# Kernel optimization log

Hardware: AMD Instinct MI355X
Metric: run time of the kernel (lower is better)

The kernel has to match this reference:

```python
import jax, jax.numpy as jnp
import numpy as np

DT = 0.02
Z_DIM = 32
U_DIM = 16


def _mlp(x, layers):
    # layers: list of (W, b); SiLU between all but last layer
    n = len(layers)
    for i, (W, b) in enumerate(layers):
        x = x @ W + b
        if i < n - 1:
            x = jax.nn.silu(x)
    return x


def _forward(x, u,
             e_w1, e_b1, e_w2, e_b2, e_w3, e_b3,
             d_w1, d_b1, d_w2, d_b2, d_w3, d_b3, d_w4, d_b4,
             a_w1, a_b1, a_w2, a_b2, a_w3, a_b3,
             b_w1, b_b1, b_w2, b_b2, b_w3, b_b3):
    # encode
    z = _mlp(x, [(e_w1, e_b1), (e_w2, e_b2), (e_w3, e_b3)])          # (B, Z)
    # state-dependent A(x) parameters: pairs (a_i, b_i) per 2x2 block
    aux = _mlp(x, [(a_w1, a_b1), (a_w2, a_b2), (a_w3, a_b3)])        # (B, Z)
    a = aux[:, 0::2]                                                  # (B, Z/2)
    b = aux[:, 1::2]
    f = jnp.exp(a * DT)
    c = jnp.cos(b * DT)
    s = jnp.sin(b * DT)
    # A(x) @ z without materializing block-diagonal: per-pair rotation-scale
    z0 = z[:, 0::2]
    z1 = z[:, 1::2]
    Az = jnp.stack([f * (c * z0 - s * z1), f * (s * z0 + c * z1)], axis=-1).reshape(z.shape)
    # B(x) @ u
    Bmat = _mlp(x, [(b_w1, b_b1), (b_w2, b_b2), (b_w3, b_b3)]).reshape(-1, Z_DIM, U_DIM)
    Bu = jnp.einsum('bzu,bu->bz', Bmat, u)
    # latent Euler step + decode
    z_next = z + DT * (Az + Bu)
    return _mlp(z_next, [(d_w1, d_b1), (d_w2, d_b2), (d_w3, d_b3), (d_w4, d_b4)])


def setup_inputs() -> dict:
    key = jax.random.key(0)
    ks = iter(jax.random.split(key, 32))
    def w(shape, scale=0.02):
        return jax.random.normal(next(ks), shape, jnp.float32) * scale
    B, X, U, Z, H, A = 16384, 64, 16, 32, 1024, 256
    return {
        'x': jax.random.normal(next(ks), (B, X), jnp.float32),
        'u': jax.random.normal(next(ks), (B, U), jnp.float32),
        'e_w1': w((X, H)), 'e_b1': w((H,)),
        'e_w2': w((H, H)), 'e_b2': w((H,)),
        'e_w3': w((H, Z)), 'e_b3': w((Z,)),
        'd_w1': w((Z, H)), 'd_b1': w((H,)),
        'd_w2': w((H, H)), 'd_b2': w((H,)),
        'd_w3': w((H, H)), 'd_b3': w((H,)),
        'd_w4': w((H, X)), 'd_b4': w((X,)),
        'a_w1': w((X, A)), 'a_b1': w((A,)),
        'a_w2': w((A, A)), 'a_b2': w((A,)),
        'a_w3': w((A, Z)), 'a_b3': w((Z,)),
        'b_w1': w((X, A)), 'b_b1': w((A,)),
        'b_w2': w((A, A)), 'b_b2': w((A,)),
        'b_w3': w((A, Z * U)), 'b_b3': w((Z * U,)),
    }


def reference(x, u,
              e_w1, e_b1, e_w2, e_b2, e_w3, e_b3,
              d_w1, d_b1, d_w2, d_b2, d_w3, d_b3, d_w4, d_b4,
              a_w1, a_b1, a_w2, a_b2, a_w3, a_b3,
              b_w1, b_b1, b_w2, b_b2, b_w3, b_b3):
    return _forward(x, u,
                    e_w1, e_b1, e_w2, e_b2, e_w3, e_b3,
                    d_w1, d_b1, d_w2, d_b2, d_w3, d_b3, d_w4, d_b4,
                    a_w1, a_b1, a_w2, a_b2, a_w3, a_b3,
                    b_w1, b_b1, b_w2, b_b2, b_w3, b_b3)
```

## Files before the change

### kernel.cpp

```cpp
#include <hip/hip_runtime.h>
#include <cstdint>
#include <cstddef>

#define B_SZ 16384
#define X_D  64
#define U_D  16
#define Z_D  32
#define H_D  1024
#define A_D  256
#define DT_C 0.02f

typedef _Float16 f16;
typedef f16   f16x8 __attribute__((ext_vector_type(8)));
typedef f16   f16x4 __attribute__((ext_vector_type(4)));
typedef float f32x4 __attribute__((ext_vector_type(4)));
typedef float f32x16 __attribute__((ext_vector_type(16)));

#define AS1 __attribute__((address_space(1)))
#define AS3 __attribute__((address_space(3)))

__device__ __forceinline__ void gld_lds16(const void* g, void* l) {
    __builtin_amdgcn_global_load_lds((AS1 void*)(g), (AS3 void*)(l), 16, 0, 0);
}

#define BARX()  do { asm volatile("" ::: "memory"); __builtin_amdgcn_s_barrier(); \
                     asm volatile("" ::: "memory"); } while (0)
#define LGK0()  do { asm volatile("s_waitcnt lgkmcnt(0)" ::: "memory"); \
                     __builtin_amdgcn_sched_barrier(0); } while (0)
#define WAITV0() asm volatile("s_waitcnt vmcnt(0)" ::: "memory")

struct GArg {
    const f16*  A;
    const f16*  W;
    const float* bias;
    void*       C;
    int lda, ldc, K;
};
struct GSet { GArg g[3]; int yn0, yn1; };

template<int BM,int BN,int BK,int WM,int WN,bool SILU,int OM>
__launch_bounds__(256)
__global__ void gemm_k(GSet p)
{
    static_assert(OM != 1 || BN == 128, "OM1 repack assumes BN=128");
    int yb = blockIdx.y, gi = 0;
    if (yb >= p.yn0) { yb -= p.yn0; gi = 1; if (yb >= p.yn1) { yb -= p.yn1; gi = 2; } }
    const GArg ga = p.g[gi];

    constexpr int SEGROW = BK / 8;
    constexpr int SMASK  = (SEGROW < 8 ? SEGROW : 8) - 1;
    constexpr int WTM = BM / WM, WTN = BN / WN;
    static_assert(WTM % 32 == 0 && WTN % 32 == 0, "wave tile in 32x32 units");
    constexpr int RM = WTM / 32, RN = WTN / 32;
    constexpr int KS = BK / 16;
    constexpr int ITA = (BM * SEGROW) / 256;
    constexpr int ITB = (BN * SEGROW) / 256;

    constexpr int STAGE_B = (BM + BN) * BK * 2;
    constexpr int CS_B    = (OM == 1) ? BM * BN * 2 : 0;
    constexpr int SMEM_B  = STAGE_B > CS_B ? STAGE_B : CS_B;
    __shared__ __align__(16) char smem[SMEM_B];
    f16* As = (f16*)smem;
    f16* Bs = As + BM * BK;

    const int tid  = threadIdx.x;
    const int lane = tid & 63;
    const int wave = tid >> 6;
    const int wm = wave / WN, wn = wave % WN;
    const int l31 = lane & 31, half = lane >> 5;

    const size_t arow0 = (size_t)blockIdx.x * BM;
    const size_t brow0 = (size_t)yb * BN;
    const int lda = ga.lda, K = ga.K;

    const f16* aptr[ITA];
    const f16* bptr[ITB];
#pragma unroll
    for (int it = 0; it < ITA; ++it) {
        int s = it * 256 + tid;
        int row = s / SEGROW, st = s % SEGROW;
        int sg = st ^ (row & SMASK);
        aptr[it] = ga.A + (arow0 + row) * lda + sg * 8;
    }
#pragma unroll
    for (int it = 0; it < ITB; ++it) {
        int s = it * 256 + tid;
        int row = s / SEGROW, st = s % SEGROW;
        int sg = st ^ (row & SMASK);
        bptr[it] = ga.W + (brow0 + row) * K + sg * 8;
    }

    f32x16 acc[RM][RN];
#pragma unroll
    for (int i = 0; i < RM; ++i)
#pragma unroll
        for (int j = 0; j < RN; ++j)
#pragma unroll
            for (int r = 0; r < 16; ++r) acc[i][j][r] = 0.f;

    for (int k0 = 0; k0 < K; k0 += BK) {
#pragma unroll
        for (int it = 0; it < ITA; ++it) {
            gld_lds16(aptr[it], &As[(it * 256 + tid) * 8]);
            aptr[it] += BK;
        }
#pragma unroll
        for (int it = 0; it < ITB; ++it) {
            gld_lds16(bptr[it], &Bs[(it * 256 + tid) * 8]);
            bptr[it] += BK;
        }
        __syncthreads();

#pragma unroll
        for (int ks = 0; ks < KS; ++ks) {
            f16x8 af[RM], bf[RN];
#pragma unroll
            for (int i = 0; i < RM; ++i) {
                int row = wm * WTM + i * 32 + l31;
                int st  = (ks * 2 + half) ^ (row & SMASK);
                af[i] = *(const f16x8*)&As[(row * SEGROW + st) * 8];
            }
#pragma unroll
            for (int j = 0; j < RN; ++j) {
                int row = wn * WTN + j * 32 + l31;
                int st  = (ks * 2 + half) ^ (row & SMASK);
                bf[j] = *(const f16x8*)&Bs[(row * SEGROW + st) * 8];
            }
#pragma unroll
            for (int i = 0; i < RM; ++i)
#pragma unroll
                for (int j = 0; j < RN; ++j)
                    acc[i][j] = __builtin_amdgcn_mfma_f32_32x32x16_f16(
                        af[i], bf[j], acc[i][j], 0, 0, 0);
        }
        __syncthreads();
    }

    const int rowbL = wm * WTM;
    const int colbL = wn * WTN;

    if constexpr (OM == 1) {
        f16* Cs = (f16*)smem;
#pragma unroll
        for (int j = 0; j < RN; ++j) {
            int colL = colbL + j * 32 + l31;
            float bv = ga.bias[(int)brow0 + colL];
            int chL = colL >> 3, wi = colL & 7;
#pragma unroll
            for (int i = 0; i < RM; ++i) {
#pragma unroll
                for (int r = 0; r < 16; ++r) {
                    int rowL = rowbL + i * 32 + (r & 3) + 8 * (r >> 2) + 4 * half;
                    float v = acc[i][j][r] + bv;
                    if (SILU) v = v / (1.0f + __expf(-v));
                    Cs[rowL * BN + ((chL ^ (rowL & 15)) << 3) + wi] = (f16)v;
                }
            }
        }
        __syncthreads();
        f16* Cout = (f16*)ga.C;
#pragma unroll
        for (int pass = 0; pass < (BM * BN / 8) / 256; ++pass) {
            int s = pass * 256 + tid;
            int rowL = s >> 4;
            int ch = s & 15;
            f16x8 v = *(const f16x8*)&Cs[rowL * BN + ((ch ^ (rowL & 15)) << 3)];
            *(f16x8*)&Cout[(size_t)(arow0 + rowL) * ga.ldc + brow0 + ch * 8] = v;
        }
    } else {
        float* Cout = (float*)ga.C;
#pragma unroll
        for (int j = 0; j < RN; ++j) {
            int col = (int)brow0 + colbL + j * 32 + l31;
            float bv = ga.bias[col];
#pragma unroll
            for (int i = 0; i < RM; ++i) {
#pragma unroll
                for (int r = 0; r < 16; ++r) {
                    int row = (int)arow0 + rowbL + i * 32
                            + (r & 3) + 8 * (r >> 2) + 4 * half;
                    float v = acc[i][j][r] + bv;
                    if (SILU) v = v / (1.0f + __expf(-v));
                    Cout[(size_t)row * ga.ldc + col] = v;
                }
            }
        }
    }
}

template<bool SILU>
__launch_bounds__(512, 2)
__global__ void gemm10_k(GSet p)
{
    int yb = blockIdx.y, gi = 0;
    if (yb >= p.yn0) { yb -= p.yn0; gi = 1; if (yb >= p.yn1) { yb -= p.yn1; gi = 2; } }
    const GArg ga = p.g[gi];

    __shared__ __align__(16) char smem[131072];

    const int tid  = threadIdx.x;
    const int lane = tid & 63, wave = tid >> 6;
    const int wm = wave >> 2, wn = wave & 3;
    const int l15 = lane & 15, quad = lane >> 4;

    const size_t arow0 = (size_t)blockIdx.x * 256;
    const size_t brow0 = (size_t)yb * 256;
    const int lda = ga.lda, K = ga.K;
    const int nt = K >> 6;

    const f16* spA[4];
    const f16* spB[4];
#pragma unroll
    for (int q = 0; q < 4; ++q) {
        int s = q * 512 + tid;
        int row = s >> 3;
        int kseg = (s & 7) ^ (row & 7);
        spA[q] = ga.A + (arow0 + row) * lda + kseg * 8;
        spB[q] = ga.W + (brow0 + row) * K + kseg * 8;
    }

    f32x4 acc[8][4];
#pragma unroll
    for (int i = 0; i < 8; ++i)
#pragma unroll
        for (int j = 0; j < 4; ++j)
#pragma unroll
            for (int r = 0; r < 4; ++r) acc[i][j][r] = 0.f;

    auto stageA = [&](char* buf, int q) {
        gld_lds16(spA[q], buf + (size_t)(q * 512 + tid) * 16);
        spA[q] += 64;
    };
    auto stageB = [&](char* buf, int q) {
        gld_lds16(spB[q], buf + 32768 + (size_t)(q * 512 + tid) * 16);
        spB[q] += 64;
    };

    f16x8 af[4][2], bf[2][2];
    auto readA = [&](const char* buf, int mh) {
#pragma unroll
        for (int i = 0; i < 4; ++i) {
            int ar = wm * 128 + mh * 64 + i * 16 + l15;
#pragma unroll
            for (int ks = 0; ks < 2; ++ks) {
                int st = (ks * 4 + quad) ^ (ar & 7);
                af[i][ks] = *(const f16x8*)(buf + ar * 128 + st * 16);
            }
        }
    };
    auto readB = [&](const char* buf, int nh) {
#pragma unroll
        for (int j = 0; j < 2; ++j) {
            int br = wn * 64 + nh * 32 + j * 16 + l15;
#pragma unroll
            for (int ks = 0; ks < 2; ++ks) {
                int st = (ks * 4 + quad) ^ (br & 7);
                bf[j][ks] = *(const f16x8*)(buf + 32768 + br * 128 + st * 16);
            }
        }
    };
    auto mma = [&](int mh, int nh) {
        __builtin_amdgcn_s_setprio(1);
#pragma unroll
        for (int ks = 0; ks < 2; ++ks)
#pragma unroll
            for (int i = 0; i < 4; ++i)
#pragma unroll
                for (int j = 0; j < 2; ++j)
                    acc[mh * 4 + i][nh * 2 + j] =
                        __builtin_amdgcn_mfma_f32_16x16x32_f16(
                            af[i][ks], bf[j][ks], acc[mh * 4 + i][nh * 2 + j],
                            0, 0, 0);
        __builtin_amdgcn_s_setprio(0);
    };

    {
        char* b0 = smem;
        stageB(b0, 0); stageB(b0, 1); stageB(b0, 2); stageB(b0, 3);
        stageA(b0, 0); stageA(b0, 1); stageA(b0, 2); stageA(b0, 3);
        WAITV0();
        BARX();
    }

    for (int t = 0; t < nt; ++t) {
        char* buf  = smem + (size_t)(t & 1) * 65536;
        char* nbuf = smem + (size_t)((t & 1) ^ 1) * 65536;
        const bool st = (t + 1 < nt);
        readA(buf, 0); readB(buf, 0);
        if (st) { stageB(nbuf, 0); stageB(nbuf, 1); stageB(nbuf, 2); stageB(nbuf, 3); }
        BARX(); LGK0(); mma(0, 0); BARX();
        readB(buf, 1);
        if (st) { stageA(nbuf, 0); stageA(nbuf, 1); stageA(nbuf, 2); stageA(nbuf, 3); }
        BARX(); LGK0(); mma(0, 1); BARX();
        readA(buf, 1);
        BARX(); LGK0(); mma(1, 1); BARX();
        readB(buf, 0);
        if (st) WAITV0();
        BARX(); LGK0(); mma(1, 0); BARX();
    }

    f16* Cs = (f16*)smem;
#pragma unroll
    for (int mf = 0; mf < 8; ++mf)
#pragma unroll
        for (int nf = 0; nf < 4; ++nf) {
            int colL = wn * 64 + (nf >> 1) * 32 + (nf & 1) * 16 + l15;
            float bv = ga.bias[(int)brow0 + colL];
            int ch = colL >> 3, wi = colL & 7;
#pragma unroll
            for (int r = 0; r < 4; ++r) {
                int rowL = wm * 128 + (mf >> 2) * 64 + (mf & 3) * 16 + quad * 4 + r;
                float v = acc[mf][nf][r] + bv;
                if (SILU) v = v / (1.0f + __expf(-v));
                Cs[rowL * 256 + ((ch ^ (rowL & 31)) << 3) + wi] = (f16)v;
            }
        }
    __syncthreads();
    f16* Cout = (f16*)ga.C;
#pragma unroll
    for (int pass = 0; pass < 16; ++pass) {
        int s = pass * 512 + tid;
        int rowL = s >> 5, ch = s & 31;
        f16x8 v = *(const f16x8*)&Cs[rowL * 256 + ((ch ^ (rowL & 31)) << 3)];
        *(f16x8*)&Cout[(size_t)(arow0 + rowL) * ga.ldc + brow0 + ch * 8] = v;
    }
}

__launch_bounds__(256)
__global__ void mid_k(const f16* __restrict__ cc2,
                      const f16* __restrict__ e_w3t, const float* __restrict__ e_b3,
                      const f16* __restrict__ a_w3t, const float* __restrict__ a_b3,
                      const f16* __restrict__ b_w3t, const float* __restrict__ b_b3,
                      const f16* __restrict__ d_w1t, const float* __restrict__ d_b1,
                      const float* __restrict__ u,   f16* __restrict__ h1d)
{
    __shared__ __align__(16) f16 As[32 * 64];
    __shared__ __align__(16) f16 Bs[128 * 64];
    __shared__ __align__(16) f16 zs[32 * 32];
    __shared__ float zb[32 * 32];
    __shared__ float ab[32 * 32];
    __shared__ float bu[32 * 32];
    __shared__ float ub[32 * 16];

    const int tid  = threadIdx.x;
    const int lane = tid & 63, wave = tid >> 6;
    const int l15 = lane & 15, quad = lane >> 4;
    const int r0 = blockIdx.x * 32;

    ub[tid]       = u[r0 * 16 + tid];
    ub[tid + 256] = u[r0 * 16 + 256 + tid];

    auto stage_d1 = [&](int ch) {
#pragma unroll
        for (int q = 0; q < 4; ++q) {
            int s = q * 256 + tid;
            int row = s >> 2, j = s & 3;
            int kseg = j ^ (row & 3);
            gld_lds16(d_w1t + (size_t)(ch * 256 + row) * 32 + kseg * 8,
                      &Bs[s * 8]);
        }
    };

#pragma unroll 1
    for (int ph = 0; ph < 2; ++ph) {
        const f16* W    = ph ? a_w3t : e_w3t;
        const float* bs = ph ? a_b3 : e_b3;
        const int K     = ph ? 256 : 1024;
        const int co    = ph ? 1024 : 0;
        float* ob       = ph ? ab : zb;
        f32x4 acc = {0.f, 0.f, 0.f, 0.f};
        for (int k0 = 0; k0 < K; k0 += 64) {
            {
                int row = tid >> 3, sg = (tid & 7) ^ (row & 7);
                gld_lds16(cc2 + (size_t)(r0 + row) * 1536 + co + k0 + sg * 8,
                          &As[tid * 8]);
            }
            {
                int row = tid >> 3, sg = (tid & 7) ^ (row & 7);
                gld_lds16(W + (size_t)row * K + k0 + sg * 8, &Bs[tid * 8]);
            }
            __syncthreads();
#pragma unroll
            for (int kk = 0; kk < 64; kk += 32) {
                int ar = ((wave >> 1) << 4) + l15;
                int ast = ((kk >> 3) + quad) ^ (ar & 7);
                f16x8 af = *(const f16x8*)&As[(ar * 8 + ast) * 8];
                int br = ((wave & 1) << 4) + l15;
                int bst = ((kk >> 3) + quad) ^ (br & 7);
                f16x8 bf = *(const f16x8*)&Bs[(br * 8 + bst) * 8];
                acc = __builtin_amdgcn_mfma_f32_16x16x32_f16(af, bf, acc, 0, 0, 0);
            }
            __syncthreads();
        }
#pragma unroll
        for (int r = 0; r < 4; ++r) {
            int row = ((wave >> 1) << 4) + quad * 4 + r;
            int col = ((wave & 1) << 4) + l15;
            ob[row * 32 + col] = acc[r] + bs[col];
        }
    }

#pragma unroll 1
    for (int ch = 0; ch < 4; ++ch) {
        f32x4 acc[2][2];
#pragma unroll
        for (int i = 0; i < 2; ++i)
#pragma unroll
            for (int j = 0; j < 2; ++j) acc[i][j] = f32x4{0.f, 0.f, 0.f, 0.f};
        for (int k0 = 0; k0 < 256; k0 += 64) {
            {   int row = tid >> 3, sg = (tid & 7) ^ (row & 7);
                gld_lds16(cc2 + (size_t)(r0 + row) * 1536 + 1280 + k0 + sg * 8,
                          &As[tid * 8]);
            }
#pragma unroll
            for (int it = 0; it < 4; ++it) {
                int s = it * 256 + tid;
                int row = s >> 3, sg = (s & 7) ^ (row & 7);
                gld_lds16(b_w3t + (size_t)(ch * 128 + row) * 256 + k0 + sg * 8,
                          &Bs[s * 8]);
            }
            __syncthreads();
#pragma unroll
            for (int kk = 0; kk < 64; kk += 32) {
                f16x8 af[2], bf[2];
#pragma unroll
                for (int i = 0; i < 2; ++i) {
                    int ar = i * 16 + l15;
                    int st = ((kk >> 3) + quad) ^ (ar & 7);
                    af[i] = *(const f16x8*)&As[(ar * 8 + st) * 8];
                }
#pragma unroll
                for (int j = 0; j < 2; ++j) {
                    int br = wave * 32 + j * 16 + l15;
                    int st = ((kk >> 3) + quad) ^ (br & 7);
                    bf[j] = *(const f16x8*)&Bs[(br * 8 + st) * 8];
                }
#pragma unroll
                for (int i = 0; i < 2; ++i)
#pragma unroll
                    for (int j = 0; j < 2; ++j)
                        acc[i][j] = __builtin_amdgcn_mfma_f32_16x16x32_f16(
                            af[i], bf[j], acc[i][j], 0, 0, 0);
            }
            __syncthreads();
        }
#pragma unroll
        for (int j = 0; j < 2; ++j) {
            int colg = ch * 128 + wave * 32 + j * 16 + l15;
            float bv = b_b3[colg];
            int z = colg >> 4;
#pragma unroll
            for (int i = 0; i < 2; ++i) {
#pragma unroll
                for (int r = 0; r < 4; ++r) {
                    int row = i * 16 + quad * 4 + r;
                    float v = (acc[i][j][r] + bv) * ub[row * 16 + l15];
                    v += __shfl_xor(v, 8, 16);
                    v += __shfl_xor(v, 4, 16);
                    v += __shfl_xor(v, 2, 16);
                    v += __shfl_xor(v, 1, 16);
                    if (l15 == 0) bu[row * 32 + z] = v;
                }
            }
        }
    }
    __syncthreads();

    stage_d1(0);
#pragma unroll
    for (int t = 0; t < 4; ++t) {
        int idx = t * 256 + tid;
        int row = idx >> 5, z = idx & 31;
        int pb = idx & ~1;
        float a  = ab[pb], b = ab[pb + 1];
        float z0 = zb[pb], z1 = zb[pb + 1];
        float f  = __expf(a * DT_C);
        float c_ = __cosf(b * DT_C);
        float s_ = __sinf(b * DT_C);
        float Az = (z & 1) ? f * (s_ * z0 + c_ * z1) : f * (c_ * z0 - s_ * z1);
        float zc = (z & 1) ? z1 : z0;
        f16 zv = (f16)(zc + DT_C * (Az + bu[idx]));
        zs[(row * 4 + ((z >> 3) ^ (row & 3))) * 8 + (z & 7)] = zv;
    }
    __syncthreads();

    f16x8 afD[2];
#pragma unroll
    for (int i = 0; i < 2; ++i) {
        int ar = i * 16 + l15;
        int ast = quad ^ (ar & 3);
        afD[i] = *(const f16x8*)&zs[(ar * 4 + ast) * 8];
    }
#pragma unroll 1
    for (int ch = 0; ch < 4; ++ch) {
        f32x4 accd[2][4];
#pragma unroll
        for (int n = 0; n < 4; ++n) {
            int br = wave * 64 + n * 16 + l15;
            int bst = quad ^ (br & 3);
            f16x8 bf = *(const f16x8*)&Bs[(br * 4 + bst) * 8];
#pragma unroll
            for (int i = 0; i < 2; ++i) {
                f32x4 zero = {0.f, 0.f, 0.f, 0.f};
                accd[i][n] = __builtin_amdgcn_mfma_f32_16x16x32_f16(
                    afD[i], bf, zero, 0, 0, 0);
            }
        }
        __syncthreads();
        if (ch < 3) stage_d1(ch + 1);
#pragma unroll
        for (int n = 0; n < 4; ++n) {
            int col = ch * 256 + wave * 64 + n * 16 + l15;
            float bv = d_b1[col];
#pragma unroll
            for (int i = 0; i < 2; ++i)
#pragma unroll
                for (int r = 0; r < 4; ++r) {
                    int row = i * 16 + quad * 4 + r;
                    float v = accd[i][n][r] + bv;
                    v = v / (1.0f + __expf(-v));
                    h1d[(size_t)(r0 + row) * 1024 + col] = (f16)v;
                }
        }
        if (ch < 3) __syncthreads();
    }
}

struct PrepArgs {
    const float* w[13];
    f16*         wt[13];
    int          K[13];
    int          N[13];
    const float* bsrc[3];
    float*       bias1;
    const float* x;
    f16*         xb;
};

__launch_bounds__(256)
__global__ void prep_k(PrepArgs pa, int ntrans, int ncvt)
{
    int bid = blockIdx.x;
    if (bid < ntrans) {
        int i = 0, t;
        for (;; ++i) {
            t = (pa.K[i] >> 5) * (pa.N[i] >> 5);
            if (bid < t) break;
            bid -= t;
        }
        const int K = pa.K[i], N = pa.N[i];
        const int tn = N >> 5;
        const int k0 = (bid / tn) << 5, n0 = (bid % tn) << 5;
        __shared__ float tbuf[32][33];
        const int tx = threadIdx.x & 31, ty = threadIdx.x >> 5;
        const float* src = pa.w[i];
        f16* dst = pa.wt[i];
#pragma unroll
        for (int r = 0; r < 32; r += 8)
            tbuf[ty + r][tx] = src[(size_t)(k0 + ty + r) * N + n0 + tx];
        __syncthreads();
#pragma unroll
        for (int r = 0; r < 32; r += 8)
            dst[(size_t)(n0 + ty + r) * K + k0 + tx] = (f16)tbuf[tx][ty + r];
    } else if (bid < ntrans + ncvt) {
        int i = ((bid - ntrans) * 256 + threadIdx.x) * 4;
        float4 v = *(const float4*)(pa.x + i);
        f16x4 o = {(f16)v.x, (f16)v.y, (f16)v.z, (f16)v.w};
        *(f16x4*)(pa.xb + i) = o;
    } else {
        int idx = (bid - ntrans - ncvt) * 256 + (int)threadIdx.x;
        float v = (idx < 1024) ? pa.bsrc[0][idx]
                : (idx < 1280) ? pa.bsrc[1][idx - 1024]
                               : pa.bsrc[2][idx - 1280];
        pa.bias1[idx] = v;
    }
}

extern "C" void kernel_launch(void* const* d_in, const int* in_sizes, int n_in,
                              void* d_out, int out_size, void* d_ws, size_t ws_size,
                              hipStream_t stream)
{
    (void)in_sizes; (void)n_in; (void)out_size; (void)ws_size;
    const float* x    = (const float*)d_in[0];
    const float* u    = (const float*)d_in[1];
    const float* e_w1 = (const float*)d_in[2];  const float* e_b1 = (const float*)d_in[3];
    const float* e_w2 = (const float*)d_in[4];  const float* e_b2 = (const float*)d_in[5];
    const float* e_w3 = (const float*)d_in[6];  const float* e_b3 = (const float*)d_in[7];
    const float* d_w1 = (const float*)d_in[8];  const float* d_b1 = (const float*)d_in[9];
    const float* d_w2 = (const float*)d_in[10]; const float* d_b2 = (const float*)d_in[11];
    const float* d_w3 = (const float*)d_in[12]; const float* d_b3 = (const float*)d_in[13];
    const float* d_w4 = (const float*)d_in[14]; const float* d_b4 = (const float*)d_in[15];
    const float* a_w1 = (const float*)d_in[16]; const float* a_b1 = (const float*)d_in[17];
    const float* a_w2 = (const float*)d_in[18]; const float* a_b2 = (const float*)d_in[19];
    const float* a_w3 = (const float*)d_in[20]; const float* a_b3 = (const float*)d_in[21];
    const float* b_w1 = (const float*)d_in[22]; const float* b_b1 = (const float*)d_in[23];
    const float* b_w2 = (const float*)d_in[24]; const float* b_b2 = (const float*)d_in[25];
    const float* b_w3 = (const float*)d_in[26]; const float* b_b3 = (const float*)d_in[27];

    char* p = (char*)d_ws;
    auto alloc = [&](size_t nbytes) -> void* {
        void* r = (void*)p;
        p += (nbytes + 255) & ~(size_t)255;
        return r;
    };
    f16*   xb   = (f16*)  alloc((size_t)B_SZ * X_D * 2);
    f16*   cc1  = (f16*)  alloc((size_t)B_SZ * 1536 * 2);
    f16*   cc2  = (f16*)  alloc((size_t)B_SZ * 1536 * 2);
    f16*   h1d  = cc1;
    f16*   h2d  = cc2;
    f16*   h3d  = cc1;
    f16*   W1t   = (f16*)alloc((size_t)1536 * X_D * 2);
    float* bias1 = (float*)alloc(1536 * 4);
    f16* e_w2t = (f16*)alloc((size_t)H_D * H_D * 2);
    f16* e_w3t = (f16*)alloc((size_t)Z_D * H_D * 2);
    f16* d_w1t = (f16*)alloc((size_t)H_D * Z_D * 2);
    f16* d_w2t = (f16*)alloc((size_t)H_D * H_D * 2);
    f16* d_w3t = (f16*)alloc((size_t)H_D * H_D * 2);
    f16* d_w4t = (f16*)alloc((size_t)X_D * H_D * 2);
    f16* a_w2t = (f16*)alloc((size_t)A_D * A_D * 2);
    f16* a_w3t = (f16*)alloc((size_t)Z_D * A_D * 2);
    f16* b_w2t = (f16*)alloc((size_t)A_D * A_D * 2);
    f16* b_w3t = (f16*)alloc((size_t)(Z_D * U_D) * A_D * 2);

    PrepArgs pa;
    const float* ws_[13] = {e_w1, e_w2, e_w3, d_w1, d_w2, d_w3, d_w4,
                            a_w1, a_w2, a_w3, b_w1, b_w2, b_w3};
    f16* wts_[13] = {W1t, e_w2t, e_w3t, d_w1t, d_w2t, d_w3t, d_w4t,
                     W1t + (size_t)1024 * X_D, a_w2t, a_w3t,
                     W1t + (size_t)1280 * X_D, b_w2t, b_w3t};
    int Ks_[13] = {X_D, H_D, H_D, Z_D, H_D, H_D, H_D, X_D, A_D, A_D, X_D, A_D, A_D};
    int Ns_[13] = {H_D, H_D, Z_D, H_D, H_D, H_D, X_D, A_D, A_D, Z_D, A_D, A_D, Z_D*U_D};
    int ntrans = 0;
    for (int i = 0; i < 13; ++i) {
        pa.w[i] = ws_[i]; pa.wt[i] = wts_[i]; pa.K[i] = Ks_[i]; pa.N[i] = Ns_[i];
        ntrans += (Ks_[i] >> 5) * (Ns_[i] >> 5);
    }
    pa.bsrc[0] = e_b1; pa.bsrc[1] = a_b1; pa.bsrc[2] = b_b1;
    pa.bias1 = bias1; pa.x = x; pa.xb = xb;
    const int ncvt = (B_SZ * X_D) / 1024;
    prep_k<<<ntrans + ncvt + 6, 256, 0, stream>>>(pa, ntrans, ncvt);

    auto G = [](const f16* A, const f16* W, const float* bias, void* C,
                int lda, int ldc, int K) {
        GArg g; g.A = A; g.W = W; g.bias = bias; g.C = C;
        g.lda = lda; g.ldc = ldc; g.K = K; return g;
    };
    GSet s;

    s.g[0] = G(xb, W1t, bias1, cc1, X_D, 1536, X_D);
    s.yn0 = 12; s.yn1 = 0;
    gemm_k<128,128,64,2,2,true,1><<<dim3(B_SZ/128, 12), 256, 0, stream>>>(s);

    s.g[0] = G(cc1,        e_w2t, e_b2, cc2,        1536, 1536, H_D);
    s.g[1] = G(cc1 + 1024, a_w2t, a_b2, cc2 + 1024, 1536, 1536, A_D);
    s.g[2] = G(cc1 + 1280, b_w2t, b_b2, cc2 + 1280, 1536, 1536, A_D);
    s.yn0 = 4; s.yn1 = 1;
    gemm10_k<true><<<dim3(B_SZ/256, 6), 512, 0, stream>>>(s);

    mid_k<<<B_SZ/32, 256, 0, stream>>>(cc2, e_w3t, e_b3, a_w3t, a_b3,
                                       b_w3t, b_b3, d_w1t, d_b1, u, h1d);

    s.yn0 = 4; s.yn1 = 0;
    s.g[0] = G(h1d, d_w2t, d_b2, h2d, H_D, H_D, H_D);
    gemm10_k<true><<<dim3(B_SZ/256, 4), 512, 0, stream>>>(s);

    s.g[0] = G(h2d, d_w3t, d_b3, h3d, H_D, H_D, H_D);
    gemm10_k<true><<<dim3(B_SZ/256, 4), 512, 0, stream>>>(s);

    s.g[0] = G(h3d, d_w4t, d_b4, d_out, H_D, X_D, H_D);
    s.yn0 = 1;
    gemm_k<64,64,64,2,2,false,0><<<dim3(B_SZ/64, 1), 256, 0, stream>>>(s);
}
```

Baseline: 347.8 us.

## Fuse final decoder layer into d_w3 GEMM via last-block atomic tail

Removes the separate final 1024->64 GEMM launch. Each 256-row block of the d_w3 GEMM increments a per-row-block atomic counter, and the last of the four column blocks to finish loads d_w4t into LDS and computes the output rows from the freshly written h3 with MFMA. This saves one kernel launch and the gap between launches. In exchange the tail work is serialized onto one block per row strip, and it relies on threadfence and atomic ordering for correctness.

```diff
diff --git a/kernel.cpp b/kernel.cpp
--- a/kernel.cpp
+++ b/kernel.cpp
@@ -38,6 +38,13 @@
 };
 struct GSet { GArg g[3]; int yn0, yn1; };
 
+struct D4Tail {
+    const f16*  w4t;
+    const float* b4;
+    float*      out;
+    int*        cnt;
+};
+
 template<int BM,int BN,int BK,int WM,int WN,bool SILU,int OM>
 __launch_bounds__(256)
 __global__ void gemm_k(GSet p)
@@ -188,9 +195,9 @@
     }
 }
 
-template<bool SILU>
+template<bool SILU, bool TAIL>
 __launch_bounds__(512, 2)
-__global__ void gemm10_k(GSet p)
+__global__ void gemm10_k(GSet p, D4Tail ta)
 {
     int yb = blockIdx.y, gi = 0;
     if (yb >= p.yn0) { yb -= p.yn0; gi = 1; if (yb >= p.yn1) { yb -= p.yn1; gi = 2; } }
@@ -324,6 +331,73 @@
         f16x8 v = *(const f16x8*)&Cs[rowL * 256 + ((ch ^ (rowL & 31)) << 3)];
         *(f16x8*)&Cout[(size_t)(arow0 + rowL) * ga.ldc + brow0 + ch * 8] = v;
     }
+
+    if constexpr (TAIL) {
+        __threadfence();
+        __syncthreads();
+        if (tid == 0) {
+            int prev = atomicAdd(ta.cnt + blockIdx.x, 1);
+            *(volatile int*)smem = (prev == 3) ? 1 : 0;
+        }
+        __syncthreads();
+        int last = *(volatile int*)smem;
+        if (!last) return;
+        __threadfence();
+
+        __syncthreads();
+#pragma unroll
+        for (int q = 0; q < 16; ++q) {
+            int s = q * 512 + tid;
+            int row = s >> 7, sl = s & 127;
+            int ssrc = (sl & ~7) | ((sl & 7) ^ (row & 7));
+            gld_lds16(ta.w4t + (size_t)row * 1024 + ssrc * 8,
+                      smem + (size_t)s * 16);
+        }
+        WAITV0();
+        BARX();
+
+        const size_t xr0 = (size_t)blockIdx.x * 256 + (size_t)wave * 32;
+        const f16* hbase = (const f16*)ga.C + xr0 * 1024;
+        f32x4 accd[2][4];
+#pragma unroll
+        for (int i = 0; i < 2; ++i)
+#pragma unroll
+            for (int n = 0; n < 4; ++n)
+#pragma unroll
+                for (int r = 0; r < 4; ++r) accd[i][n][r] = 0.f;
+
+        for (int ks = 0; ks < 32; ++ks) {
+            int k0 = ks * 32;
+            f16x8 afr[2];
+#pragma unroll
+            for (int i = 0; i < 2; ++i)
+                afr[i] = *(const f16x8*)&hbase[(size_t)(i * 16 + l15) * 1024
+                                               + k0 + quad * 8];
+#pragma unroll
+            for (int n = 0; n < 4; ++n) {
+                int col = n * 16 + l15;
+                int slot = (k0 >> 3) + quad;
+                int sl2 = (slot & ~7) | ((slot & 7) ^ (col & 7));
+                f16x8 bfr = *(const f16x8*)(smem + (size_t)col * 2048 + sl2 * 16);
+#pragma unroll
+                for (int i = 0; i < 2; ++i)
+                    accd[i][n] = __builtin_amdgcn_mfma_f32_16x16x32_f16(
+                        afr[i], bfr, accd[i][n], 0, 0, 0);
+            }
+        }
+#pragma unroll
+        for (int n = 0; n < 4; ++n) {
+            int col = n * 16 + l15;
+            float bv = ta.b4[col];
+#pragma unroll
+            for (int i = 0; i < 2; ++i)
+#pragma unroll
+                for (int r = 0; r < 4; ++r) {
+                    size_t row = xr0 + i * 16 + quad * 4 + r;
+                    ta.out[row * 64 + col] = accd[i][n][r] + bv;
+                }
+        }
+    }
 }
 
 __launch_bounds__(256)
@@ -535,6 +609,7 @@
     float*       bias1;
     const float* x;
     f16*         xb;
+    int*         cnt;
 };
 
 __launch_bounds__(256)
@@ -573,6 +648,7 @@
                 : (idx < 1280) ? pa.bsrc[1][idx - 1024]
                                : pa.bsrc[2][idx - 1280];
         pa.bias1[idx] = v;
+        if (idx < 64) pa.cnt[idx] = 0;
     }
 }
 
@@ -621,6 +697,7 @@
     f16* a_w3t = (f16*)alloc((size_t)Z_D * A_D * 2);
     f16* b_w2t = (f16*)alloc((size_t)A_D * A_D * 2);
     f16* b_w3t = (f16*)alloc((size_t)(Z_D * U_D) * A_D * 2);
+    int* d4cnt = (int*)alloc(64 * 4);
 
     PrepArgs pa;
     const float* ws_[13] = {e_w1, e_w2, e_w3, d_w1, d_w2, d_w3, d_w4,
@@ -636,7 +713,7 @@
         ntrans += (Ks_[i] >> 5) * (Ns_[i] >> 5);
     }
     pa.bsrc[0] = e_b1; pa.bsrc[1] = a_b1; pa.bsrc[2] = b_b1;
-    pa.bias1 = bias1; pa.x = x; pa.xb = xb;
+    pa.bias1 = bias1; pa.x = x; pa.xb = xb; pa.cnt = d4cnt;
     const int ncvt = (B_SZ * X_D) / 1024;
     prep_k<<<ntrans + ncvt + 6, 256, 0, stream>>>(pa, ntrans, ncvt);
 
@@ -646,6 +723,7 @@
         g.lda = lda; g.ldc = ldc; g.K = K; return g;
     };
     GSet s;
+    D4Tail tz{};
 
     s.g[0] = G(xb, W1t, bias1, cc1, X_D, 1536, X_D);
     s.yn0 = 12; s.yn1 = 0;
@@ -655,19 +733,17 @@
     s.g[1] = G(cc1 + 1024, a_w2t, a_b2, cc2 + 1024, 1536, 1536, A_D);
     s.g[2] = G(cc1 + 1280, b_w2t, b_b2, cc2 + 1280, 1536, 1536, A_D);
     s.yn0 = 4; s.yn1 = 1;
-    gemm10_k<true><<<dim3(B_SZ/256, 6), 512, 0, stream>>>(s);
+    gemm10_k<true,false><<<dim3(B_SZ/256, 6), 512, 0, stream>>>(s, tz);
 
     mid_k<<<B_SZ/32, 256, 0, stream>>>(cc2, e_w3t, e_b3, a_w3t, a_b3,
                                        b_w3t, b_b3, d_w1t, d_b1, u, h1d);
 
     s.yn0 = 4; s.yn1 = 0;
     s.g[0] = G(h1d, d_w2t, d_b2, h2d, H_D, H_D, H_D);
-    gemm10_k<true><<<dim3(B_SZ/256, 4), 512, 0, stream>>>(s);
+    gemm10_k<true,false><<<dim3(B_SZ/256, 4), 512, 0, stream>>>(s, tz);
 
     s.g[0] = G(h2d, d_w3t, d_b3, h3d, H_D, H_D, H_D);
-    gemm10_k<true><<<dim3(B_SZ/256, 4), 512, 0, stream>>>(s);
-
-    s.g[0] = G(h3d, d_w4t, d_b4, d_out, H_D, X_D, H_D);
-    s.yn0 = 1;
-    gemm_k<64,64,64,2,2,false,0><<<dim3(B_SZ/64, 1), 256, 0, stream>>>(s);
+    D4Tail ta;
+    ta.w4t = d_w4t; ta.b4 = d_b4; ta.out = (float*)d_out; ta.cnt = d4cnt;
+    gemm10_k<true,true><<<dim3(B_SZ/256, 4), 512, 0, stream>>>(s, ta);
 }
```

Measured after the change: 421.6 us. +21.2%, slower.

## Add 128x256-tile triple-buffered GEMM kernel for the fused second layer

Applied to the files above, without the earlier changes.

Adds a new GEMM kernel that uses a 128-row by 256-column tile with a three-stage LDS ring buffer fed by direct global-to-LDS loads, and uses it only for the grouped second hidden layer (encoder, A-net and B-net). Halving the M tile doubles the grid, which is meant to improve load balance and occupancy for the smaller K=256 groups. The triple buffering with partial vmcnt waits aims to hide load latency better. The cost is more LDS (144KB) and less reuse of the A operand per block.

```diff
diff --git a/kernel.cpp b/kernel.cpp
--- a/kernel.cpp
+++ b/kernel.cpp
@@ -27,6 +27,7 @@
                      asm volatile("" ::: "memory"); } while (0)
 #define LGK0()  do { asm volatile("s_waitcnt lgkmcnt(0)" ::: "memory"); \
                      __builtin_amdgcn_sched_barrier(0); } while (0)
+#define WAITV6() asm volatile("s_waitcnt vmcnt(6)" ::: "memory")
 #define WAITV0() asm volatile("s_waitcnt vmcnt(0)" ::: "memory")
 
 struct GArg {
@@ -185,6 +186,143 @@
                 }
             }
         }
+    }
+}
+
+template<bool SILU>
+__launch_bounds__(512, 2)
+__global__ void gemm9_k(GSet p)
+{
+    int yb = blockIdx.y, gi = 0;
+    if (yb >= p.yn0) { yb -= p.yn0; gi = 1; if (yb >= p.yn1) { yb -= p.yn1; gi = 2; } }
+    const GArg ga = p.g[gi];
+
+    __shared__ __align__(16) char smem[147456];
+
+    const int tid  = threadIdx.x;
+    const int lane = tid & 63, wave = tid >> 6;
+    const int wm = wave >> 2, wn = wave & 3;
+    const int l15 = lane & 15, quad = lane >> 4;
+    const int r7  = l15 & 7;
+
+    const size_t arow0 = (size_t)blockIdx.x * 128;
+    const size_t brow0 = (size_t)yb * 256;
+    const int lda = ga.lda, K = ga.K;
+    const int nt = K >> 6;
+
+    const f16* spA[2];
+    const f16* spB[4];
+#pragma unroll
+    for (int q = 0; q < 2; ++q) {
+        int s = q * 512 + tid;
+        int urow = s >> 3;
+        int kseg = (s & 7) ^ (urow & 7);
+        spA[q] = ga.A + (arow0 + urow) * lda + kseg * 8;
+    }
+#pragma unroll
+    for (int q = 0; q < 4; ++q) {
+        int s = q * 512 + tid;
+        int urow = s >> 3;
+        int kseg = (s & 7) ^ (urow & 7);
+        spB[q] = ga.W + (brow0 + urow) * K + kseg * 8;
+    }
+
+    f32x4 acc[4][4];
+#pragma unroll
+    for (int i = 0; i < 4; ++i)
+#pragma unroll
+        for (int j = 0; j < 4; ++j)
+#pragma unroll
+            for (int r = 0; r < 4; ++r) acc[i][j][r] = 0.f;
+
+    auto stageA = [&](char* buf, int q) {
+        gld_lds16(spA[q], buf + (size_t)(q * 512 + tid) * 16);
+        spA[q] += 64;
+    };
+    auto stageB = [&](char* buf, int q) {
+        gld_lds16(spB[q], buf + 16384 + (size_t)(q * 512 + tid) * 16);
+        spB[q] += 64;
+    };
+
+    f16x8 af[4], bf[4];
+    auto readAB = [&](const char* buf, int ks) {
+        int slot = (((ks << 2) | quad) ^ r7) * 16;
+#pragma unroll
+        for (int f = 0; f < 4; ++f) {
+            int row = wm * 64 + f * 16 + l15;
+            af[f] = *(const f16x8*)(buf + row * 128 + slot);
+        }
+#pragma unroll
+        for (int f = 0; f < 4; ++f) {
+            int row = wn * 64 + f * 16 + l15;
+            bf[f] = *(const f16x8*)(buf + 16384 + row * 128 + slot);
+        }
+    };
+    auto mma = [&]() {
+        __builtin_amdgcn_s_setprio(1);
+#pragma unroll
+        for (int f = 0; f < 4; ++f)
+#pragma unroll
+            for (int n = 0; n < 4; ++n)
+                acc[f][n] = __builtin_amdgcn_mfma_f32_16x16x32_f16(
+                    af[f], bf[n], acc[f][n], 0, 0, 0);
+        __builtin_amdgcn_s_setprio(0);
+    };
+
+    {
+        char* b0 = smem;
+        char* b1 = smem + 49152;
+        stageB(b0, 0); stageB(b0, 1); stageB(b0, 2); stageB(b0, 3);
+        stageA(b0, 0); stageA(b0, 1);
+        stageB(b1, 0); stageB(b1, 1); stageB(b1, 2); stageB(b1, 3);
+        stageA(b1, 0); stageA(b1, 1);
+        WAITV6();
+        BARX();
+    }
+
+    int bi = 0;
+    for (int t = 0; t < nt; ++t) {
+        char* buf = smem + bi * 49152;
+        int nxi = bi + 2; if (nxi >= 3) nxi -= 3;
+        char* nbuf = smem + nxi * 49152;
+        const bool st = (t + 2 < nt);
+        readAB(buf, 0);
+        if (st) { stageB(nbuf, 0); stageB(nbuf, 1); stageB(nbuf, 2); stageB(nbuf, 3); }
+        BARX(); LGK0();
+        mma();
+        readAB(buf, 1);
+        if (st) { stageA(nbuf, 0); stageA(nbuf, 1); }
+        if (st) { WAITV6(); } else if (t + 2 == nt) { WAITV0(); }
+        BARX(); LGK0();
+        mma();
+        bi += 1; if (bi >= 3) bi -= 3;
+    }
+
+    BARX();
+    f16* Cs = (f16*)smem;
+#pragma unroll
+    for (int mf = 0; mf < 4; ++mf)
+#pragma unroll
+        for (int nf = 0; nf < 4; ++nf) {
+            int colL = wn * 64 + nf * 16 + l15;
+            float bv = ga.bias[(int)brow0 + colL];
+            int ch = colL >> 3, wi = colL & 7;
+#pragma unroll
+            for (int r = 0; r < 4; ++r) {
+                int rowL = wm * 64 + mf * 16 + quad * 4 + r;
+                float v = acc[mf][nf][r] + bv;
+                if (SILU) v = v / (1.0f + __expf(-v));
+                Cs[rowL * 256 + ((ch ^ (rowL & 31)) << 3) + wi] = (f16)v;
+            }
+        }
+    __syncthreads();
+    f16* Cout = (f16*)ga.C;
+#pragma unroll
+    for (int pass = 0; pass < 8; ++pass) {
+        int s = pass * 512 + tid;
+        int rowL = s >> 5, ch = s & 31;
+        f16x8 v = *(const f16x8*)&Cs[rowL * 256 + ((ch ^ (rowL & 31)) << 3)];
+        *(f16x8*)&Cout[(size_t)(arow0 + rowL) * ga.ldc + brow0 + ch * 8] = v;
     }
 }
 
@@ -655,7 +793,7 @@
     s.g[1] = G(cc1 + 1024, a_w2t, a_b2, cc2 + 1024, 1536, 1536, A_D);
     s.g[2] = G(cc1 + 1280, b_w2t, b_b2, cc2 + 1280, 1536, 1536, A_D);
     s.yn0 = 4; s.yn1 = 1;
-    gemm10_k<true><<<dim3(B_SZ/256, 6), 512, 0, stream>>>(s);
+    gemm9_k<true><<<dim3(B_SZ/128, 6), 512, 0, stream>>>(s);
 
     mid_k<<<B_SZ/32, 256, 0, stream>>>(cc2, e_w3t, e_b3, a_w3t, a_b3,
                                        b_w3t, b_b3, d_w1t, d_b1, u, h1d);
```

Measured after the change: 362.8 us. +4.3%, slower.
